# Kernel optimization log

Measured on AMD Instinct MI355X. Metric: run time of the kernel, lower is better.

Reference implementation:

```python
import jax, jax.numpy as jnp
import numpy as np

GRID = 300  # NaiveFourierKANLayer default gridsize
EPS = 1e-5


def layer_norm(x, w, b):
    mu = jnp.mean(x, axis=-1, keepdims=True)
    var = jnp.var(x, axis=-1, keepdims=True)
    return (x - mu) * jax.lax.rsqrt(var + EPS) * w + b


def fourier_kan(x, coeffs, bias):
    # x: [..., I], coeffs: [2, O, I, G], bias: [1, O]
    shp = x.shape
    I = shp[-1]
    xf = x.reshape(-1, I)
    k = jnp.arange(1, GRID + 1, dtype=x.dtype)           # [G]
    arg = xf[:, :, None] * k                             # [B, I, G]
    y = jnp.einsum('big,oig->bo', jnp.cos(arg), coeffs[0])
    y = y + jnp.einsum('big,oig->bo', jnp.sin(arg), coeffs[1])
    y = y + bias                                         # bias broadcasts [1, O]
    return y.reshape(shp[:-1] + (coeffs.shape[1],))


def setup_inputs() -> dict:
    key = jax.random.key(0)
    ks = jax.random.split(key, 4)
    B, N, D = 8, 196, 128          # batch, in_channels, in_dim
    O1 = 2 * D                     # amplifier out_dim
    x = jax.random.normal(ks[0], (B, N, D), dtype=jnp.float32)
    fc1_coeffs = jax.random.normal(ks[1], (2, O1, D, GRID), dtype=jnp.float32) / np.sqrt(D * GRID)
    fc2_coeffs = jax.random.normal(ks[2], (2, N, N, GRID), dtype=jnp.float32) / np.sqrt(N * GRID)
    return {
        'x': x,
        'ln1_w': jnp.ones((D,), jnp.float32),
        'ln1_b': jnp.zeros((D,), jnp.float32),
        'fc1_coeffs': fc1_coeffs,
        'fc1_bias': jnp.zeros((1, O1), jnp.float32),
        'ln2_w': jnp.ones((O1,), jnp.float32),
        'ln2_b': jnp.zeros((O1,), jnp.float32),
        'fc2_coeffs': fc2_coeffs,
        'fc2_bias': jnp.zeros((1, N), jnp.float32),
    }


def reference(x, ln1_w, ln1_b, fc1_coeffs, fc1_bias, ln2_w, ln2_b, fc2_coeffs, fc2_bias):
    B, N, D = x.shape
    # amplifier: LN over in_dim, FourierKAN in_dim -> 2*in_dim
    h = fourier_kan(layer_norm(x, ln1_w, ln1_b), fc1_coeffs, fc1_bias)   # [B, N, 2D]
    # channel_mix: LN over 2*in_dim, transpose, FourierKAN over channels, transpose back
    h = layer_norm(h, ln2_w, ln2_b)
    h = jnp.transpose(h, (0, 2, 1))                                      # [B, 2D, N]
    h = fourier_kan(h, fc2_coeffs, fc2_bias)                             # [B, 2D, N]
    h = jnp.transpose(h, (0, 2, 1))                                      # [B, N, 2D]
    return h.reshape(-1, 2 * N, D)                                       # [B, 2N, D]
```

## Files before the change

### kernel.cpp

```cpp
#include <hip/hip_runtime.h>
#include <math.h>

typedef short short8 __attribute__((ext_vector_type(8)));
typedef float f32x4 __attribute__((ext_vector_type(4)));

#define EPSF 1e-5f

union FragU { uint4 q; unsigned u[4]; short8 v; };

__device__ __forceinline__ unsigned pack_trunc2(float lo_val, float hi_val) {
    return __builtin_amdgcn_perm(__float_as_uint(hi_val), __float_as_uint(lo_val), 0x07060302u);
}
__device__ __forceinline__ float trunc_bf(float x) {
    return __uint_as_float(__float_as_uint(x) & 0xFFFF0000u);
}

__global__ void ln1_kernel(const float* __restrict__ x, const float* __restrict__ w,
                           const float* __restrict__ b, float* __restrict__ xnT) {
    int r = blockIdx.x;
    int t = threadIdx.x;
    const float* row = x + (size_t)r * 128;
    float v0 = row[t], v1 = row[t + 64];
    float s = v0 + v1, q = v0 * v0 + v1 * v1;
    #pragma unroll
    for (int off = 32; off > 0; off >>= 1) {
        s += __shfl_down(s, off);
        q += __shfl_down(q, off);
    }
    s = __shfl(s, 0); q = __shfl(q, 0);
    float mu = s * (1.f / 128.f);
    float var = q * (1.f / 128.f) - mu * mu;
    float rs = rsqrtf(var + EPSF);
    xnT[(size_t)t * 1792 + r]        = (v0 - mu) * rs * w[t]      + b[t];
    xnT[(size_t)(t + 64) * 1792 + r] = (v1 - mu) * rs * w[t + 64] + b[t + 64];
}

__launch_bounds__(256)
__global__ void fc1_kernel(const float* __restrict__ xnT, const float* __restrict__ coeffs,
                           float* __restrict__ h1, int KS) {
    const int nt = blockIdx.x;
    const int mt = blockIdx.y;
    const int ks = blockIdx.z;
    const int i0 = (ks * 128) / KS, i1 = ((ks + 1) * 128) / KS;
    const int t = threadIdx.x;
    const int wv = t >> 6, ln = t & 63;
    const int q = ln >> 4, col = ln & 15;
    const int mwrow = mt * 256 + wv * 64;

    __shared__ unsigned bhi[128 * 36];
    __shared__ unsigned blo[128 * 36];

    const float* c0 = coeffs;
    const float* c1 = coeffs + (size_t)256 * 128 * 300;

    f32x4 acc[4][8] = {};

    const int srow = t >> 1;
    const int j0 = (t & 1) * 16;
    const int og = nt * 128 + srow;
    const size_t prow = (size_t)og * 128;

    for (int i = i0; i < i1; ++i) {
        float zu[4];
        #pragma unroll
        for (int mf = 0; mf < 4; ++mf) {
            int m = mwrow + mf * 16 + col;
            zu[mf] = (m < 1568) ? xnT[(size_t)i * 1792 + m] : 0.f;
        }
        const float* p0 = c0 + (prow + i) * 300;
        const float* p1 = c1 + (prow + i) * 300;

        for (int c = 0; c < 10; ++c) {
            __syncthreads();
            {
                unsigned hw[16], lw[16];
                #pragma unroll
                for (int k4 = 0; k4 < 4; ++k4) {
                    int g = c * 32 + j0 + k4 * 4;
                    float w0[4], w1[4];
                    if (g + 4 <= 300) {
                        float4 a = *(const float4*)(p0 + g);
                        float4 bb = *(const float4*)(p1 + g);
                        w0[0]=a.x; w0[1]=a.y; w0[2]=a.z; w0[3]=a.w;
                        w1[0]=bb.x; w1[1]=bb.y; w1[2]=bb.z; w1[3]=bb.w;
                    } else {
                        #pragma unroll
                        for (int e = 0; e < 4; ++e) {
                            int gg = g + e; bool ok = gg < 300;
                            w0[e] = ok ? p0[gg] : 0.f;
                            w1[e] = ok ? p1[gg] : 0.f;
                        }
                    }
                    #pragma unroll
                    for (int e = 0; e < 4; ++e) {
                        hw[k4*4+e] = pack_trunc2(w0[e], w1[e]);
                        lw[k4*4+e] = pack_trunc2(w0[e]-trunc_bf(w0[e]), w1[e]-trunc_bf(w1[e]));
                    }
                }
                int base = srow * 36 + j0;
                *(uint4*)&bhi[base]      = make_uint4(hw[0], hw[1], hw[2], hw[3]);
                *(uint4*)&bhi[base + 4]  = make_uint4(hw[4], hw[5], hw[6], hw[7]);
                *(uint4*)&bhi[base + 8]  = make_uint4(hw[8], hw[9], hw[10], hw[11]);
                *(uint4*)&bhi[base + 12] = make_uint4(hw[12], hw[13], hw[14], hw[15]);
                *(uint4*)&blo[base]      = make_uint4(lw[0], lw[1], lw[2], lw[3]);
                *(uint4*)&blo[base + 4]  = make_uint4(lw[4], lw[5], lw[6], lw[7]);
                *(uint4*)&blo[base + 8]  = make_uint4(lw[8], lw[9], lw[10], lw[11]);
                *(uint4*)&blo[base + 12] = make_uint4(lw[12], lw[13], lw[14], lw[15]);
            }
            __syncthreads();
            #pragma unroll
            for (int h = 0; h < 2; ++h) {
                FragU ah[4], al[4];
                #pragma unroll
                for (int mf = 0; mf < 4; ++mf) {
                    #pragma unroll
                    for (int d = 0; d < 4; ++d) {
                        float kf = (float)(c * 32 + h * 16 + q * 4 + d + 1);
                        float a = zu[mf] * kf;
                        float cv = __cosf(a), sv = __sinf(a);
                        ah[mf].u[d] = pack_trunc2(cv, sv);
                        al[mf].u[d] = pack_trunc2(cv - trunc_bf(cv), sv - trunc_bf(sv));
                    }
                }
                #pragma unroll
                for (int nf = 0; nf < 8; ++nf) {
                    int addr = (nf * 16 + col) * 36 + h * 16 + q * 4;
                    FragU bh, bl;
                    bh.q = *(const uint4*)&bhi[addr];
                    bl.q = *(const uint4*)&blo[addr];
                    #pragma unroll
                    for (int mf = 0; mf < 4; ++mf) {
                        acc[mf][nf] = __builtin_amdgcn_mfma_f32_16x16x32_bf16(ah[mf].v, bh.v, acc[mf][nf], 0, 0, 0);
                        acc[mf][nf] = __builtin_amdgcn_mfma_f32_16x16x32_bf16(ah[mf].v, bl.v, acc[mf][nf], 0, 0, 0);
                        acc[mf][nf] = __builtin_amdgcn_mfma_f32_16x16x32_bf16(al[mf].v, bh.v, acc[mf][nf], 0, 0, 0);
                    }
                }
            }
        }
    }
    #pragma unroll
    for (int mf = 0; mf < 4; ++mf) {
        if (mwrow + mf * 16 >= 1568) continue;
        int mbase = mwrow + mf * 16 + q * 4;
        #pragma unroll
        for (int nf = 0; nf < 8; ++nf) {
            int o = nt * 128 + nf * 16 + col;
            #pragma unroll
            for (int r = 0; r < 4; ++r)
                atomicAdd(&h1[(size_t)(mbase + r) * 256 + o], acc[mf][nf][r]);
        }
    }
}

__global__ void ln2_kernel(const float* __restrict__ h1, const float* __restrict__ bias,
                           const float* __restrict__ w, const float* __restrict__ b,
                           float* __restrict__ h1n) {
    int r = blockIdx.x;
    int t = threadIdx.x;
    float v = h1[(size_t)r * 256 + t] + bias[t];
    float s = v, q = v * v;
    #pragma unroll
    for (int off = 32; off > 0; off >>= 1) {
        s += __shfl_down(s, off);
        q += __shfl_down(q, off);
    }
    __shared__ float ss[4], qq[4];
    int wid = t >> 6;
    if ((t & 63) == 0) { ss[wid] = s; qq[wid] = q; }
    __syncthreads();
    float S = ss[0] + ss[1] + ss[2] + ss[3];
    float Q = qq[0] + qq[1] + qq[2] + qq[3];
    float mu = S * (1.f / 256.f);
    float var = Q * (1.f / 256.f) - mu * mu;
    float rs = rsqrtf(var + EPSF);
    h1n[(size_t)r * 256 + t] = (v - mu) * rs * w[t] + b[t];
}

__device__ __forceinline__ void cmul(float& xr, float& xi, float br, float bi) {
    float nr = xr * br - xi * bi;
    float ni = xr * bi + xi * br;
    xr = nr; xi = ni;
}

__launch_bounds__(256)
__global__ void fc2_kernel(const float* __restrict__ h1n, const float* __restrict__ coeffs,
                           float* __restrict__ out, int KS) {
    const int nt = blockIdx.x;
    const int b  = blockIdx.y;
    const int ks = blockIdx.z;
    const int i0 = (ks * 196) / KS, i1 = ((ks + 1) * 196) / KS;
    const int t = threadIdx.x;
    const int wv = t >> 6, ln = t & 63;
    const int q = ln >> 4, col = ln & 15;
    const int cwb = wv * 64;

    __shared__ unsigned bs[128 * 36];

    const float* d0 = coeffs;
    const float* d1 = coeffs + (size_t)196 * 196 * 300;

    f32x4 acc[4][8] = {};

    const int srow = t >> 1;
    const int j0 = (t & 1) * 16;
    const int og = nt * 128 + srow;
    const bool son = (og < 196);
    const size_t prow = (size_t)og * 196;

    for (int i = i0; i < i1; ++i) {
        float Rc[4], Rs[4], E1c[4], E1s[4], E13c[4], E13s[4];
        #pragma unroll
        for (int mf = 0; mf < 4; ++mf) {
            float x = h1n[((size_t)b * 196 + i) * 256 + cwb + mf * 16 + col];
            float c1_ = __cosf(x), s1_ = __sinf(x);
            float c2 = c1_*c1_ - s1_*s1_, s2 = 2.f*c1_*s1_;
            float c4 = c2*c2 - s2*s2,    s4 = 2.f*c2*s2;
            float c8 = c4*c4 - s4*s4,    s8 = 2.f*c4*s4;
            float c12 = c8*c4 - s8*s4,   s12 = c8*s4 + s8*c4;
            float c13 = c12*c1_ - s12*s1_, s13 = c12*s1_ + s12*c1_;
            float rc = c1_, rs = s1_;
            float m4c = (q & 1) ? c4 : 1.f, m4s = (q & 1) ? s4 : 0.f;
            cmul(rc, rs, m4c, m4s);
            float m8c = (q & 2) ? c8 : 1.f, m8s = (q & 2) ? s8 : 0.f;
            cmul(rc, rs, m8c, m8s);
            Rc[mf] = rc; Rs[mf] = rs;
            E1c[mf] = c1_; E1s[mf] = s1_;
            E13c[mf] = c13; E13s[mf] = s13;
        }
        const float* p0 = d0 + prow * 300 + (size_t)i * 300;
        const float* p1 = d1 + prow * 300 + (size_t)i * 300;

        for (int c = 0; c < 10; ++c) {
            __syncthreads();
            {
                unsigned hw[16];
                #pragma unroll
                for (int k4 = 0; k4 < 4; ++k4) {
                    int g = c * 32 + j0 + k4 * 4;
                    float w0[4], w1[4];
                    if (son && g + 4 <= 300) {
                        float4 a = *(const float4*)(p0 + g);
                        float4 bb = *(const float4*)(p1 + g);
                        w0[0]=a.x; w0[1]=a.y; w0[2]=a.z; w0[3]=a.w;
                        w1[0]=bb.x; w1[1]=bb.y; w1[2]=bb.z; w1[3]=bb.w;
                    } else {
                        #pragma unroll
                        for (int e = 0; e < 4; ++e) {
                            int gg = g + e; bool ok = son && (gg < 300);
                            w0[e] = ok ? p0[gg] : 0.f;
                            w1[e] = ok ? p1[gg] : 0.f;
                        }
                    }
                    #pragma unroll
                    for (int e = 0; e < 4; ++e) hw[k4*4+e] = pack_trunc2(w0[e], w1[e]);
                }
                int base = srow * 36 + j0;
                *(uint4*)&bs[base]      = make_uint4(hw[0], hw[1], hw[2], hw[3]);
                *(uint4*)&bs[base + 4]  = make_uint4(hw[4], hw[5], hw[6], hw[7]);
                *(uint4*)&bs[base + 8]  = make_uint4(hw[8], hw[9], hw[10], hw[11]);
                *(uint4*)&bs[base + 12] = make_uint4(hw[12], hw[13], hw[14], hw[15]);
            }
            __syncthreads();
            #pragma unroll
            for (int h = 0; h < 2; ++h) {
                FragU af[4];
                #pragma unroll
                for (int mf = 0; mf < 4; ++mf) {
                    #pragma unroll
                    for (int d = 0; d < 4; ++d) {
                        af[mf].u[d] = pack_trunc2(Rc[mf], Rs[mf]);
                        if (d < 3) cmul(Rc[mf], Rs[mf], E1c[mf], E1s[mf]);
                        else       cmul(Rc[mf], Rs[mf], E13c[mf], E13s[mf]);
                    }
                }
                #pragma unroll
                for (int nf = 0; nf < 8; ++nf) {
                    int addr = (nf * 16 + col) * 36 + h * 16 + q * 4;
                    FragU bf;
                    bf.q = *(const uint4*)&bs[addr];
                    #pragma unroll
                    for (int mf = 0; mf < 4; ++mf)
                        acc[mf][nf] = __builtin_amdgcn_mfma_f32_16x16x32_bf16(af[mf].v, bf.v, acc[mf][nf], 0, 0, 0);
                }
            }
        }
    }
    #pragma unroll
    for (int mf = 0; mf < 4; ++mf) {
        int cbase = cwb + mf * 16 + q * 4;
        #pragma unroll
        for (int nf = 0; nf < 8; ++nf) {
            int o = nt * 128 + nf * 16 + col;
            if (o < 196) {
                #pragma unroll
                for (int r = 0; r < 4; ++r)
                    atomicAdd(&out[((size_t)b * 196 + o) * 256 + cbase + r], acc[mf][nf][r]);
            }
        }
    }
}

__global__ void bias2_kernel(float* __restrict__ out, const float* __restrict__ bias) {
    int idx = blockIdx.x * 256 + threadIdx.x;
    int o = (idx >> 8) % 196;
    out[idx] += bias[o];
}

extern "C" void kernel_launch(void* const* d_in, const int* in_sizes, int n_in,
                              void* d_out, int out_size, void* d_ws, size_t ws_size,
                              hipStream_t stream) {
    const float* x       = (const float*)d_in[0];
    const float* ln1w    = (const float*)d_in[1];
    const float* ln1b    = (const float*)d_in[2];
    const float* fc1c    = (const float*)d_in[3];
    const float* fc1bias = (const float*)d_in[4];
    const float* ln2w    = (const float*)d_in[5];
    const float* ln2b    = (const float*)d_in[6];
    const float* fc2c    = (const float*)d_in[7];
    const float* fc2bias = (const float*)d_in[8];
    float* out = (float*)d_out;

    float* xnT = (float*)d_ws;
    float* h1  = xnT + 229376;
    float* h1n = h1 + 401408;

    hipMemsetAsync(h1, 0, (size_t)401408 * 4, stream);
    hipMemsetAsync(d_out, 0, (size_t)401408 * 4, stream);

    const int ks1 = 32, ks2 = 28;
    ln1_kernel<<<1568, 64, 0, stream>>>(x, ln1w, ln1b, xnT);
    fc1_kernel<<<dim3(2, 7, ks1), 256, 0, stream>>>(xnT, fc1c, h1, ks1);
    ln2_kernel<<<1568, 256, 0, stream>>>(h1, fc1bias, ln2w, ln2b, h1n);
    fc2_kernel<<<dim3(2, 8, ks2), 256, 0, stream>>>(h1n, fc2c, out, ks2);
    bias2_kernel<<<1568, 256, 0, stream>>>(out, fc2bias);
}
```

Measured before the change: 742.5 us.

## Double-buffer fc2 coefficient tiles and prefetch next chunk into registers

The fc2 kernel now keeps two LDS buffers for the packed bf16 coefficient tile and issues the global loads for the next chunk right after storing the current one, so global latency overlaps the MFMA work. The two barriers per chunk become one custom lgkmcnt wait plus s_barrier, and s_setprio raises wave priority around the MFMA section. This costs more LDS and 32 extra prefetch registers per thread, which may lower occupancy. Correctness relies on the single barrier being enough to stop the ping-pong buffers from racing.

```diff
diff --git a/kernel.cpp b/kernel.cpp
--- a/kernel.cpp
+++ b/kernel.cpp
@@ -14,6 +14,13 @@
 __device__ __forceinline__ float trunc_bf(float x) {
     return __uint_as_float(__float_as_uint(x) & 0xFFFF0000u);
 }
+
+#define LGKM0_BAR() do { \
+    asm volatile("s_waitcnt lgkmcnt(0)" ::: "memory"); \
+    __builtin_amdgcn_s_barrier(); \
+    __builtin_amdgcn_sched_barrier(0); \
+    asm volatile("" ::: "memory"); \
+} while (0)
 
 __global__ void ln1_kernel(const float* __restrict__ x, const float* __restrict__ w,
                            const float* __restrict__ b, float* __restrict__ xnT) {
@@ -194,7 +201,7 @@
     const int q = ln >> 4, col = ln & 15;
     const int cwb = wv * 64;
 
-    __shared__ unsigned bs[128 * 36];
+    __shared__ unsigned bs[2][128 * 36];
 
     const float* d0 = coeffs;
     const float* d1 = coeffs + (size_t)196 * 196 * 300;
@@ -207,6 +214,43 @@
     const bool son = (og < 196);
     const size_t prow = (size_t)og * 196;
 
+    float w0[16], w1[16];
+
+    auto LOAD = [&](int i, int c) {
+        const float* p0 = d0 + (prow + i) * 300;
+        const float* p1 = d1 + (prow + i) * 300;
+        #pragma unroll
+        for (int k4 = 0; k4 < 4; ++k4) {
+            int g = c * 32 + j0 + k4 * 4;
+            if (son && g + 4 <= 300) {
+                float4 a  = *(const float4*)(p0 + g);
+                float4 bb = *(const float4*)(p1 + g);
+                w0[k4*4+0]=a.x;  w0[k4*4+1]=a.y;  w0[k4*4+2]=a.z;  w0[k4*4+3]=a.w;
+                w1[k4*4+0]=bb.x; w1[k4*4+1]=bb.y; w1[k4*4+2]=bb.z; w1[k4*4+3]=bb.w;
+            } else {
+                #pragma unroll
+                for (int e = 0; e < 4; ++e) {
+                    int gg = g + e; bool ok = son && (gg < 300);
+                    w0[k4*4+e] = ok ? p0[gg] : 0.f;
+                    w1[k4*4+e] = ok ? p1[gg] : 0.f;
+                }
+            }
+        }
+    };
+
+    auto PACKSTORE = [&](int buf) {
+        unsigned hw[16];
+        #pragma unroll
+        for (int e = 0; e < 16; ++e) hw[e] = pack_trunc2(w0[e], w1[e]);
+        int base = srow * 36 + j0;
+        *(uint4*)&bs[buf][base]      = make_uint4(hw[0],  hw[1],  hw[2],  hw[3]);
+        *(uint4*)&bs[buf][base + 4]  = make_uint4(hw[4],  hw[5],  hw[6],  hw[7]);
+        *(uint4*)&bs[buf][base + 8]  = make_uint4(hw[8],  hw[9],  hw[10], hw[11]);
+        *(uint4*)&bs[buf][base + 12] = make_uint4(hw[12], hw[13], hw[14], hw[15]);
+    };
+
+    int cur = 0;
+    LOAD(i0, 0);
     for (int i = i0; i < i1; ++i) {
         float Rc[4], Rs[4], E1c[4], E1s[4], E13c[4], E13s[4];
         #pragma unroll
@@ -227,40 +271,13 @@
             E1c[mf] = c1_; E1s[mf] = s1_;
             E13c[mf] = c13; E13s[mf] = s13;
         }
-        const float* p0 = d0 + prow * 300 + (size_t)i * 300;
-        const float* p1 = d1 + prow * 300 + (size_t)i * 300;
-
         for (int c = 0; c < 10; ++c) {
-            __syncthreads();
-            {
-                unsigned hw[16];
-                #pragma unroll
-                for (int k4 = 0; k4 < 4; ++k4) {
-                    int g = c * 32 + j0 + k4 * 4;
-                    float w0[4], w1[4];
-                    if (son && g + 4 <= 300) {
-                        float4 a = *(const float4*)(p0 + g);
-                        float4 bb = *(const float4*)(p1 + g);
-                        w0[0]=a.x; w0[1]=a.y; w0[2]=a.z; w0[3]=a.w;
-                        w1[0]=bb.x; w1[1]=bb.y; w1[2]=bb.z; w1[3]=bb.w;
-                    } else {
-                        #pragma unroll
-                        for (int e = 0; e < 4; ++e) {
-                            int gg = g + e; bool ok = son && (gg < 300);
-                            w0[e] = ok ? p0[gg] : 0.f;
-                            w1[e] = ok ? p1[gg] : 0.f;
-                        }
-                    }
-                    #pragma unroll
-                    for (int e = 0; e < 4; ++e) hw[k4*4+e] = pack_trunc2(w0[e], w1[e]);
-                }
-                int base = srow * 36 + j0;
-                *(uint4*)&bs[base]      = make_uint4(hw[0], hw[1], hw[2], hw[3]);
-                *(uint4*)&bs[base + 4]  = make_uint4(hw[4], hw[5], hw[6], hw[7]);
-                *(uint4*)&bs[base + 8]  = make_uint4(hw[8], hw[9], hw[10], hw[11]);
-                *(uint4*)&bs[base + 12] = make_uint4(hw[12], hw[13], hw[14], hw[15]);
-            }
-            __syncthreads();
+            PACKSTORE(cur);
+            int ni = i, nc = c + 1;
+            if (nc == 10) { nc = 0; ni = i + 1; }
+            if (ni < i1) LOAD(ni, nc);
+            LGKM0_BAR();
+            __builtin_amdgcn_s_setprio(1);
             #pragma unroll
             for (int h = 0; h < 2; ++h) {
                 FragU af[4];
@@ -277,12 +294,14 @@
                 for (int nf = 0; nf < 8; ++nf) {
                     int addr = (nf * 16 + col) * 36 + h * 16 + q * 4;
                     FragU bf;
-                    bf.q = *(const uint4*)&bs[addr];
+                    bf.q = *(const uint4*)&bs[cur][addr];
                     #pragma unroll
                     for (int mf = 0; mf < 4; ++mf)
                         acc[mf][nf] = __builtin_amdgcn_mfma_f32_16x16x32_bf16(af[mf].v, bf.v, acc[mf][nf], 0, 0, 0);
                 }
             }
+            __builtin_amdgcn_s_setprio(0);
+            cur ^= 1;
         }
     }
     #pragma unroll
```

Measured after the change: 842.7 us. 13.5% more time.
